# Kernel tuning notes

Measured on AMD Instinct MI355X. Metric: run time of the kernel, lower is better.

## Reference

```python
import jax, jax.numpy as jnp
import numpy as np

D_MODEL = 768
N_HEADS = 12
HEAD_DIM = D_MODEL // N_HEADS


def setup_inputs() -> dict:
    key = jax.random.key(0)
    ks = jax.random.split(key, 9)
    s = 1.0 / np.sqrt(D_MODEL)
    inp = {
        "inputs": jax.random.normal(ks[0], (1, 4096, D_MODEL), dtype=jnp.float32),
        "Wq": jax.random.uniform(ks[1], (D_MODEL, D_MODEL), jnp.float32, -s, s),
        "bq": jax.random.uniform(ks[2], (D_MODEL,), jnp.float32, -s, s),
        "Wk": jax.random.uniform(ks[3], (D_MODEL, D_MODEL), jnp.float32, -s, s),
        "bk": jax.random.uniform(ks[4], (D_MODEL,), jnp.float32, -s, s),
        "Wv": jax.random.uniform(ks[5], (D_MODEL, D_MODEL), jnp.float32, -s, s),
        "bv": jax.random.uniform(ks[6], (D_MODEL,), jnp.float32, -s, s),
        "Wo": jax.random.uniform(ks[7], (D_MODEL, D_MODEL), jnp.float32, -s, s),
        "bo": jax.random.uniform(ks[8], (D_MODEL,), jnp.float32, -s, s),
    }
    return inp


def reference(inputs, Wq, bq, Wk, bk, Wv, bv, Wo, bo):
    B, S, D = inputs.shape
    H, Hd = N_HEADS, HEAD_DIM

    def split_heads(x):  # [B,S,D] -> [B,H,S,Hd]
        return x.reshape(B, S, H, Hd).transpose(0, 2, 1, 3)

    # nn.Linear computes x @ W.T + b
    Q = split_heads(inputs @ Wq.T + bq)
    K = split_heads(inputs @ Wk.T + bk)
    V = split_heads(inputs @ Wv.T + bv)

    scores = jnp.einsum("bhsd,bhtd->bhst", Q, K) / jnp.sqrt(jnp.float32(Hd))
    causal = jnp.tril(jnp.ones((S, S), dtype=bool))  # True = keep
    scores = jnp.where(causal, scores, -jnp.inf)
    attn = jax.nn.softmax(scores, axis=-1)  # dropout is identity in eval

    out = jnp.einsum("bhst,bhtd->bhsd", attn, V)
    out = out.transpose(0, 2, 1, 3).reshape(B, S, D)
    return out @ Wo.T + bo
```

## Files before the change

kernel.cpp:

```cpp
#include <hip/hip_runtime.h>
#include <stdint.h>

#define SEQ 4096
#define DM 768
#define NH 12
#define HD 64

typedef unsigned short u16;
typedef short short8 __attribute__((ext_vector_type(8)));
typedef float floatx4 __attribute__((ext_vector_type(4)));
typedef float floatx16 __attribute__((ext_vector_type(16)));
typedef u16 u16x4 __attribute__((ext_vector_type(4)));

__device__ inline u16 f2b(float f) {
  union { float f; uint32_t u; } v; v.f = f;
  uint32_t u = v.u;
  return (u16)((u + 0x7fffu + ((u >> 16) & 1u)) >> 16);
}

__device__ inline float b2f(u16 x) {
  union { uint32_t u; float f; } v; v.u = ((uint32_t)x) << 16;
  return v.f;
}

#if defined(__has_builtin)
#if __has_builtin(__builtin_amdgcn_cvt_pk_bf16_f32)
#define HAVE_PK_BF16 1
#endif
#endif

__device__ inline uint32_t pk_bf16(float a, float b) {
#ifdef HAVE_PK_BF16
  typedef __bf16 bf16x2_t __attribute__((ext_vector_type(2)));
  union { bf16x2_t v; uint32_t u; } c;
  c.v = __builtin_amdgcn_cvt_pk_bf16_f32(a, b);
  return c.u;
#else
  uint32_t r;
  asm("v_cvt_pk_bf16_f32 %0, %1, %2" : "=v"(r) : "v"(a), "v"(b));
  return r;
#endif
}

__device__ inline void pl32swap(uint32_t& a, uint32_t& b) {
  asm("v_permlane32_swap_b32 %0, %1" : "+v"(a), "+v"(b));
}

__device__ inline void load_lds16(const void* g, void* l) {
  __builtin_amdgcn_global_load_lds(
      (const __attribute__((address_space(1))) uint32_t*)g,
      (__attribute__((address_space(3))) uint32_t*)l, 16, 0, 0);
}

__global__ __launch_bounds__(256) void convert_all(
    const float* __restrict__ X, const float* __restrict__ Wq,
    const float* __restrict__ Wk, const float* __restrict__ Wv,
    const float* __restrict__ Wo,
    u16* __restrict__ Xb, u16* __restrict__ Wqb, u16* __restrict__ Wkb,
    u16* __restrict__ Wvb, u16* __restrict__ Wob) {
  int t = blockIdx.x * 256 + threadIdx.x;
  const int NX = SEQ * DM / 4;
  const int NW = DM * DM / 4;
  const float* src; u16* dst; int off;
  if (t < NX)               { src = X;  dst = Xb;  off = t; }
  else if (t < NX + NW)     { src = Wq; dst = Wqb; off = t - NX; }
  else if (t < NX + 2 * NW) { src = Wk; dst = Wkb; off = t - NX - NW; }
  else if (t < NX + 3 * NW) { src = Wv; dst = Wvb; off = t - NX - 2 * NW; }
  else if (t < NX + 4 * NW) { src = Wo; dst = Wob; off = t - NX - 3 * NW; }
  else return;
  float4 v = *(const float4*)(src + (size_t)off * 4);
  uint2 o;
  o.x = pk_bf16(v.x, v.y);
  o.y = pk_bf16(v.z, v.w);
  *(uint2*)(dst + (size_t)off * 4) = o;
}

__global__ __launch_bounds__(256) void gemm_qkv(
    const u16* __restrict__ Xb,
    const u16* __restrict__ Wqb, const u16* __restrict__ Wkb,
    const u16* __restrict__ Wvb,
    const float* __restrict__ bq, const float* __restrict__ bk,
    const float* __restrict__ bv,
    u16* __restrict__ Qh, u16* __restrict__ Kh, u16* __restrict__ VtG) {
  const u16* W; const float* bias;
  const int z = blockIdx.z;
  if (z == 0)      { W = Wqb; bias = bq; }
  else if (z == 1) { W = Wkb; bias = bk; }
  else             { W = Wvb; bias = bv; }

  __shared__ u16 smem[16384];

  const int tid = threadIdx.x;
  const int wave = tid >> 6, lane = tid & 63;
  const int g = lane >> 4, ln = lane & 15;
  const int m0 = blockIdx.y * 64, n0 = blockIdx.x * 64;
  const int wm = (wave & 1) * 32, wn = (wave >> 1) * 32;
  const int srow = lane >> 3;
  const int schunk = (lane & 7) ^ srow;
  const int swz = ln & 7;

  floatx4 acc[2][2] = {};

#pragma unroll
  for (int i = 0; i < 2; ++i) {
    int u = wave * 2 + i;
    load_lds16(Xb + (size_t)(m0 + u * 8 + srow) * DM + schunk * 8, smem + u * 512);
    load_lds16(W + (size_t)(n0 + u * 8 + srow) * DM + schunk * 8,
               smem + 8192 + u * 512);
  }

  for (int kt = 0; kt < 12; ++kt) {
    const int cur = kt & 1;
    __syncthreads();
    if (kt < 11) {
      const int k0 = (kt + 1) * 64, nb = cur ^ 1;
#pragma unroll
      for (int i = 0; i < 2; ++i) {
        int u = wave * 2 + i;
        load_lds16(Xb + (size_t)(m0 + u * 8 + srow) * DM + k0 + schunk * 8,
                   smem + nb * 4096 + u * 512);
        load_lds16(W + (size_t)(n0 + u * 8 + srow) * DM + k0 + schunk * 8,
                   smem + 8192 + nb * 4096 + u * 512);
      }
    }
    const u16* Ac = smem + cur * 4096;
    const u16* Bc = smem + 8192 + cur * 4096;
    short8 af[2][2], bf[2][2];
#pragma unroll
    for (int mi = 0; mi < 2; ++mi)
#pragma unroll
      for (int kh = 0; kh < 2; ++kh)
        af[mi][kh] = *(const short8*)(Ac + (wm + mi * 16 + ln) * 64 +
                                      ((kh * 4 + g) ^ swz) * 8);
#pragma unroll
    for (int ni = 0; ni < 2; ++ni)
#pragma unroll
      for (int kh = 0; kh < 2; ++kh)
        bf[ni][kh] = *(const short8*)(Bc + (wn + ni * 16 + ln) * 64 +
                                      ((kh * 4 + g) ^ swz) * 8);
#pragma unroll
    for (int kh = 0; kh < 2; ++kh)
#pragma unroll
      for (int mi = 0; mi < 2; ++mi)
#pragma unroll
        for (int ni = 0; ni < 2; ++ni)
          acc[mi][ni] = __builtin_amdgcn_mfma_f32_16x16x32_bf16(
              af[mi][kh], bf[ni][kh], acc[mi][ni], 0, 0, 0);
  }

  const float qscale = 0.125f * 1.44269504089f;
  const int hh = n0 >> 6;
  __syncthreads();

  if (z == 2) {
#pragma unroll
    for (int mi = 0; mi < 2; ++mi) {
      int row0 = wm + mi * 16 + g * 4;
#pragma unroll
      for (int ni = 0; ni < 2; ++ni) {
        int col = wn + ni * 16 + ln;
        float b = bias[n0 + col];
        uint2 o;
        o.x = pk_bf16(acc[mi][ni][0] + b, acc[mi][ni][1] + b);
        o.y = pk_bf16(acc[mi][ni][2] + b, acc[mi][ni][3] + b);
        *(uint2*)(smem + col * 72 + row0) = o;
      }
    }
    __syncthreads();
#pragma unroll
    for (int t = 0; t < 2; ++t) {
      int unit = tid + t * 256;
      int dcol = unit >> 3, ch = unit & 7;
      short8 v = *(const short8*)(smem + dcol * 72 + ch * 8);
      *(short8*)(VtG + ((size_t)(hh * 64 + dcol)) * SEQ + m0 + ch * 8) = v;
    }
  } else {
    u16* out = (z == 0) ? Qh : Kh;
    float cs = (z == 0) ? qscale : 1.0f;
#pragma unroll
    for (int mi = 0; mi < 2; ++mi) {
      int row0 = wm + mi * 16 + g * 4;
#pragma unroll
      for (int ni = 0; ni < 2; ++ni) {
        int col = wn + ni * 16 + ln;
        float b = bias[n0 + col];
        uint32_t w0 = pk_bf16((acc[mi][ni][0] + b) * cs, (acc[mi][ni][1] + b) * cs);
        uint32_t w1 = pk_bf16((acc[mi][ni][2] + b) * cs, (acc[mi][ni][3] + b) * cs);
        smem[(row0 + 0) * 72 + col] = (u16)w0;
        smem[(row0 + 1) * 72 + col] = (u16)(w0 >> 16);
        smem[(row0 + 2) * 72 + col] = (u16)w1;
        smem[(row0 + 3) * 72 + col] = (u16)(w1 >> 16);
      }
    }
    __syncthreads();
#pragma unroll
    for (int t = 0; t < 2; ++t) {
      int unit = tid + t * 256;
      int row = unit >> 3, ch = unit & 7;
      short8 v = *(const short8*)(smem + row * 72 + ch * 8);
      *(short8*)(out + ((size_t)hh * SEQ + m0 + row) * HD + ch * 8) = v;
    }
  }
}

#define CHUNK 8
#define M0 40.0f
__global__ __launch_bounds__(256, 4) void attn_chunk(
    const u16* __restrict__ Qh, const u16* __restrict__ Kh,
    const u16* __restrict__ VtG, u16* __restrict__ Opart,
    float* __restrict__ Lp) {
  const int p = blockIdx.y * NH + blockIdx.x;
  const int slot = p % 24, cyc = p / 24;
  const int qq = 3 * (slot & 7) + (slot >> 3);
  const int h = qq >> 1;
  const int j = cyc * 2 + (qq & 1);
  const int r = 143 - j;
  int g = 0;
#pragma unroll
  for (int t = 1; t < 8; ++t)
    if (2 * t * (t + 1) <= r) g = t;
  const int gp1 = g + 1;
  const int rr = r - 2 * g * gp1;
  const int dq = rr / gp1;
  const int qB = 4 * g + dq;
  const int ci = rr - dq * gp1;
  const int kb0 = ci * CHUNK;
  const int kb1 = min(kb0 + CHUNK, 2 * qB + 2);
  const int slot2 = h * 144 + gp1 * (2 * g + (qB & 3)) + ci;

  const int tid = threadIdx.x, wave = tid >> 6, lane = tid & 63;
  const int hi = lane >> 5, lq = lane & 31;
  const int q0 = qB * 128;
  const int qwave = q0 + wave * 32;
  const int srow = lane >> 3;
  const int schunk = (lane & 7) ^ srow;
  const int rsw = lane & 7;

  __shared__ u16 Ks[2 * 4096];
  __shared__ u16 Vt[2 * 4096];

  const int qglob = qwave + lq;
  const u16* Qbase = Qh + ((size_t)h * SEQ + qglob) * HD;
  short8 aq[4];
#pragma unroll
  for (int s = 0; s < 4; ++s)
    aq[s] = *(const short8*)(Qbase + s * 16 + hi * 8);

  floatx16 oacc[2] = {};
  floatx4 lacc = {};

  const size_t kbase = (size_t)h * SEQ * HD;
  const size_t vbase = (size_t)h * 64 * SEQ;

  auto stage = [&](int kbIdx, int buf) {
#pragma unroll
    for (int i = 0; i < 2; ++i) {
      int u = wave * 2 + i;
      load_lds16(Kh + kbase + (size_t)(kbIdx * 64 + u * 8 + srow) * HD + schunk * 8,
                 Ks + buf * 4096 + u * 512);
      load_lds16(VtG + vbase + (size_t)(u * 8 + srow) * SEQ + kbIdx * 64 + schunk * 8,
                 Vt + buf * 4096 + u * 512);
    }
  };

  stage(kb0, 0);

  for (int kb = kb0; kb < kb1; ++kb) {
    const int cur = (kb - kb0) & 1;
    __syncthreads();
    if (kb + 1 < kb1) stage(kb + 1, cur ^ 1);

    const u16* Kc = Ks + cur * 4096;
    const u16* Vc = Vt + cur * 4096;

    if (kb * 64 > qwave + 31) continue;

    floatx16 st[2];
#pragma unroll
    for (int kblk = 0; kblk < 2; ++kblk)
#pragma unroll
      for (int r2 = 0; r2 < 16; ++r2) st[kblk][r2] = -M0;
    __builtin_amdgcn_s_setprio(1);
#pragma unroll
    for (int s = 0; s < 4; ++s)
#pragma unroll
      for (int kblk = 0; kblk < 2; ++kblk) {
        short8 kf = *(const short8*)(Kc + (kblk * 32 + lq) * 64 +
                                     ((s * 2 + hi) ^ rsw) * 8);
        st[kblk] = __builtin_amdgcn_mfma_f32_32x32x16_bf16(kf, aq[s], st[kblk],
                                                           0, 0, 0);
      }
    __builtin_amdgcn_s_setprio(0);

    if (kb * 64 + 63 > qwave) {
#pragma unroll
      for (int kblk = 0; kblk < 2; ++kblk)
#pragma unroll
        for (int r2 = 0; r2 < 16; ++r2) {
          int key = kb * 64 + kblk * 32 + (r2 & 3) + 8 * (r2 >> 2) + 4 * hi;
          if (key > qglob) st[kblk][r2] = -1e30f;
        }
    }

    uint32_t w[2][8];
#pragma unroll
    for (int kblk = 0; kblk < 2; ++kblk) {
#pragma unroll
      for (int r2 = 0; r2 < 16; ++r2)
        st[kblk][r2] = __builtin_amdgcn_exp2f(st[kblk][r2]);
#pragma unroll
      for (int r2 = 0; r2 < 4; ++r2)
        lacc[r2] += st[kblk][r2] + st[kblk][4 + r2] + st[kblk][8 + r2] +
                    st[kblk][12 + r2];
#pragma unroll
      for (int i = 0; i < 8; ++i)
        w[kblk][i] = pk_bf16(st[kblk][2 * i], st[kblk][2 * i + 1]);
    }

    __builtin_amdgcn_s_setprio(1);
#pragma unroll
    for (int ks = 0; ks < 4; ++ks) {
      const int kblk = ks >> 1, base = (ks & 1) * 4;
      uint32_t d0 = w[kblk][base + 0], d2 = w[kblk][base + 2];
      uint32_t d1 = w[kblk][base + 1], d3 = w[kblk][base + 3];
      pl32swap(d0, d2);
      pl32swap(d1, d3);
      union { uint32_t u[4]; short8 s; } bp;
      bp.u[0] = d0; bp.u[1] = d1; bp.u[2] = d2; bp.u[3] = d3;
#pragma unroll
      for (int dblk = 0; dblk < 2; ++dblk) {
        short8 vf = *(const short8*)(Vc + (dblk * 32 + lq) * 64 +
                                     ((ks * 2 + hi) ^ rsw) * 8);
        oacc[dblk] = __builtin_amdgcn_mfma_f32_32x32x16_bf16(vf, bp.s, oacc[dblk],
                                                             0, 0, 0);
      }
    }
    __builtin_amdgcn_s_setprio(0);
  }

  float l_i = lacc[0] + lacc[1] + lacc[2] + lacc[3];
  l_i += __shfl_xor(l_i, 32);

  float inv = 1.f / l_i;
  int qloc = wave * 32 + lq;
  u16* Op = Opart + (size_t)slot2 * 8192 + qloc * 64;
#pragma unroll
  for (int dblk = 0; dblk < 2; ++dblk)
#pragma unroll
    for (int qd = 0; qd < 4; ++qd) {
      uint2 o;
      o.x = pk_bf16(oacc[dblk][qd * 4 + 0] * inv, oacc[dblk][qd * 4 + 1] * inv);
      o.y = pk_bf16(oacc[dblk][qd * 4 + 2] * inv, oacc[dblk][qd * 4 + 3] * inv);
      *(uint2*)(Op + dblk * 32 + qd * 8 + hi * 4) = o;
    }
  if (hi == 0) Lp[(size_t)slot2 * 128 + qloc] = l_i;
}

__global__ __launch_bounds__(256) void attn_merge(
    const u16* __restrict__ Opart, const float* __restrict__ Lp,
    u16* __restrict__ Ob) {
  const int h = blockIdx.x, qB = blockIdx.y;
  const int g = qB >> 2;
  const int n = g + 1;
  const int base = h * 144 + (g + 1) * (2 * g + (qB & 3));
  const int q = threadIdx.x >> 1;
  const int d0 = (threadIdx.x & 1) * 32;

  float L = 0.f;
  for (int i = 0; i < n; ++i) L += Lp[(size_t)(base + i) * 128 + q];
  float invL = 1.f / L;

  float acc[32];
#pragma unroll
  for (int jj = 0; jj < 32; ++jj) acc[jj] = 0.f;
  for (int i = 0; i < n; ++i) {
    float wi = Lp[(size_t)(base + i) * 128 + q] * invL;
    const u16* src = Opart + (size_t)(base + i) * 8192 + q * 64 + d0;
#pragma unroll
    for (int c = 0; c < 4; ++c) {
      short8 a = ((const short8*)src)[c];
#pragma unroll
      for (int jj = 0; jj < 8; ++jj) acc[c * 8 + jj] += wi * b2f((u16)a[jj]);
    }
  }

  u16* dst = Ob + (size_t)(qB * 128 + q) * DM + h * HD + d0;
#pragma unroll
  for (int c = 0; c < 4; ++c) {
    uint4 o;
    o.x = pk_bf16(acc[c * 8 + 0], acc[c * 8 + 1]);
    o.y = pk_bf16(acc[c * 8 + 2], acc[c * 8 + 3]);
    o.z = pk_bf16(acc[c * 8 + 4], acc[c * 8 + 5]);
    o.w = pk_bf16(acc[c * 8 + 6], acc[c * 8 + 7]);
    ((uint4*)dst)[c] = o;
  }
}

__global__ __launch_bounds__(256) void gemm_out(
    const u16* __restrict__ Ab, const u16* __restrict__ Wob,
    const float* __restrict__ bo, float* __restrict__ Cout) {
  __shared__ u16 smem[16384];

  const int tid = threadIdx.x;
  const int wave = tid >> 6, lane = tid & 63;
  const int g = lane >> 4, ln = lane & 15;
  const int m0 = blockIdx.y * 64, n0 = blockIdx.x * 64;
  const int wm = (wave & 1) * 32, wn = (wave >> 1) * 32;
  const int srow = lane >> 3;
  const int schunk = (lane & 7) ^ srow;
  const int swz = ln & 7;

  floatx4 acc[2][2] = {};

#pragma unroll
  for (int i = 0; i < 2; ++i) {
    int u = wave * 2 + i;
    load_lds16(Ab + (size_t)(m0 + u * 8 + srow) * DM + schunk * 8, smem + u * 512);
    load_lds16(Wob + (size_t)(n0 + u * 8 + srow) * DM + schunk * 8,
               smem + 8192 + u * 512);
  }

  for (int kt = 0; kt < 12; ++kt) {
    const int cur = kt & 1;
    __syncthreads();
    if (kt < 11) {
      const int k0 = (kt + 1) * 64, nb = cur ^ 1;
#pragma unroll
      for (int i = 0; i < 2; ++i) {
        int u = wave * 2 + i;
        load_lds16(Ab + (size_t)(m0 + u * 8 + srow) * DM + k0 + schunk * 8,
                   smem + nb * 4096 + u * 512);
        load_lds16(Wob + (size_t)(n0 + u * 8 + srow) * DM + k0 + schunk * 8,
                   smem + 8192 + nb * 4096 + u * 512);
      }
    }
    const u16* Ac = smem + cur * 4096;
    const u16* Bc = smem + 8192 + cur * 4096;
    short8 af[2][2], bf[2][2];
#pragma unroll
    for (int mi = 0; mi < 2; ++mi)
#pragma unroll
      for (int kh = 0; kh < 2; ++kh)
        af[mi][kh] = *(const short8*)(Ac + (wm + mi * 16 + ln) * 64 +
                                      ((kh * 4 + g) ^ swz) * 8);
#pragma unroll
    for (int ni = 0; ni < 2; ++ni)
#pragma unroll
      for (int kh = 0; kh < 2; ++kh)
        bf[ni][kh] = *(const short8*)(Bc + (wn + ni * 16 + ln) * 64 +
                                      ((kh * 4 + g) ^ swz) * 8);
#pragma unroll
    for (int kh = 0; kh < 2; ++kh)
#pragma unroll
      for (int mi = 0; mi < 2; ++mi)
#pragma unroll
        for (int ni = 0; ni < 2; ++ni)
          acc[mi][ni] = __builtin_amdgcn_mfma_f32_16x16x32_bf16(
              af[mi][kh], bf[ni][kh], acc[mi][ni], 0, 0, 0);
  }

#pragma unroll
  for (int mi = 0; mi < 2; ++mi) {
    int row = m0 + wm + mi * 16 + g * 4;
#pragma unroll
    for (int ni = 0; ni < 2; ++ni) {
      int col = n0 + wn + ni * 16 + ln;
      float b = bo[col];
#pragma unroll
      for (int r = 0; r < 4; ++r)
        Cout[(size_t)(row + r) * DM + col] = acc[mi][ni][r] + b;
    }
  }
}

extern "C" void kernel_launch(void* const* d_in, const int* in_sizes, int n_in,
                              void* d_out, int out_size, void* d_ws, size_t ws_size,
                              hipStream_t stream) {
  const float* X  = (const float*)d_in[0];
  const float* Wq = (const float*)d_in[1];
  const float* bq = (const float*)d_in[2];
  const float* Wk = (const float*)d_in[3];
  const float* bk = (const float*)d_in[4];
  const float* Wv = (const float*)d_in[5];
  const float* bv = (const float*)d_in[6];
  const float* Wo = (const float*)d_in[7];
  const float* bo = (const float*)d_in[8];
  float* out = (float*)d_out;

  char* ws = (char*)d_ws;
  u16* Wob = (u16*)ws; ws += (size_t)DM * DM * 2;
  u16* Qh  = (u16*)ws; ws += (size_t)NH * SEQ * HD * 2;
  u16* Kh  = (u16*)ws; ws += (size_t)NH * SEQ * HD * 2;
  u16* VtG = (u16*)ws; ws += (size_t)NH * SEQ * HD * 2;
  u16* Ob  = (u16*)ws; ws += (size_t)SEQ * DM * 2;
  float* Lp = (float*)ws; ws += (size_t)NH * 144 * 128 * 4;
  char* ovl = ws;
  u16* Xb  = (u16*)ovl;
  u16* Wqb = Xb + (size_t)SEQ * DM;
  u16* Wkb = Wqb + (size_t)DM * DM;
  u16* Wvb = Wkb + (size_t)DM * DM;
  u16* Opart = (u16*)ovl;

  convert_all<<<5376, 256, 0, stream>>>(X, Wq, Wk, Wv, Wo, Xb, Wqb, Wkb, Wvb, Wob);

  dim3 gq(DM / 64, SEQ / 64, 3);
  gemm_qkv<<<gq, 256, 0, stream>>>(Xb, Wqb, Wkb, Wvb, bq, bk, bv, Qh, Kh, VtG);

  dim3 ga(NH, 144);
  attn_chunk<<<ga, 256, 0, stream>>>(Qh, Kh, VtG, Opart, Lp);

  dim3 gm(NH, 32);
  attn_merge<<<gm, 256, 0, stream>>>(Opart, Lp, Ob);

  dim3 go(DM / 64, SEQ / 64);
  gemm_out<<<go, 256, 0, stream>>>(Ob, Wob, bo, out);
}
```

Baseline: 175.8 us.

## Enlarge GEMM tiles to 128x64 with 2 waves and double attention key chunk

```diff
diff --git a/kernel.cpp b/kernel.cpp
--- a/kernel.cpp
+++ b/kernel.cpp
@@ -10,7 +10,6 @@
 typedef short short8 __attribute__((ext_vector_type(8)));
 typedef float floatx4 __attribute__((ext_vector_type(4)));
 typedef float floatx16 __attribute__((ext_vector_type(16)));
-typedef u16 u16x4 __attribute__((ext_vector_type(4)));
 
 __device__ inline u16 f2b(float f) {
   union { float f; uint32_t u; } v; v.f = f;
@@ -75,7 +74,7 @@
   *(uint2*)(dst + (size_t)off * 4) = o;
 }
 
-__global__ __launch_bounds__(256) void gemm_qkv(
+__global__ __launch_bounds__(128) void gemm_qkv(
     const u16* __restrict__ Xb,
     const u16* __restrict__ Wqb, const u16* __restrict__ Wkb,
     const u16* __restrict__ Wvb,
@@ -88,122 +87,120 @@
   else if (z == 1) { W = Wkb; bias = bk; }
   else             { W = Wvb; bias = bv; }
 
-  __shared__ u16 smem[16384];
+  __shared__ u16 As[2 * 8192];
+  __shared__ u16 Bs[2 * 4096];
 
   const int tid = threadIdx.x;
   const int wave = tid >> 6, lane = tid & 63;
   const int g = lane >> 4, ln = lane & 15;
-  const int m0 = blockIdx.y * 64, n0 = blockIdx.x * 64;
-  const int wm = (wave & 1) * 32, wn = (wave >> 1) * 32;
+  const int m0 = blockIdx.y * 128, n0 = blockIdx.x * 64;
   const int srow = lane >> 3;
   const int schunk = (lane & 7) ^ srow;
   const int swz = ln & 7;
 
-  floatx4 acc[2][2] = {};
-
-#pragma unroll
-  for (int i = 0; i < 2; ++i) {
-    int u = wave * 2 + i;
-    load_lds16(Xb + (size_t)(m0 + u * 8 + srow) * DM + schunk * 8, smem + u * 512);
-    load_lds16(W + (size_t)(n0 + u * 8 + srow) * DM + schunk * 8,
-               smem + 8192 + u * 512);
-  }
+  floatx4 acc[4][4] = {};
+
+  auto stage = [&](int k0, int buf) {
+#pragma unroll
+    for (int i = 0; i < 8; ++i) {
+      int u = wave * 8 + i;
+      load_lds16(Xb + (size_t)(m0 + u * 8 + srow) * DM + k0 + schunk * 8,
+                 As + buf * 8192 + u * 512);
+    }
+#pragma unroll
+    for (int i = 0; i < 4; ++i) {
+      int u = wave * 4 + i;
+      load_lds16(W + (size_t)(n0 + u * 8 + srow) * DM + k0 + schunk * 8,
+                 Bs + buf * 4096 + u * 512);
+    }
+  };
+
+  stage(0, 0);
 
   for (int kt = 0; kt < 12; ++kt) {
     const int cur = kt & 1;
     __syncthreads();
-    if (kt < 11) {
-      const int k0 = (kt + 1) * 64, nb = cur ^ 1;
-#pragma unroll
-      for (int i = 0; i < 2; ++i) {
-        int u = wave * 2 + i;
-        load_lds16(Xb + (size_t)(m0 + u * 8 + srow) * DM + k0 + schunk * 8,
-                   smem + nb * 4096 + u * 512);
-        load_lds16(W + (size_t)(n0 + u * 8 + srow) * DM + k0 + schunk * 8,
-                   smem + 8192 + nb * 4096 + u * 512);
-      }
-    }
-    const u16* Ac = smem + cur * 4096;
-    const u16* Bc = smem + 8192 + cur * 4096;
-    short8 af[2][2], bf[2][2];
-#pragma unroll
-    for (int mi = 0; mi < 2; ++mi)
-#pragma unroll
-      for (int kh = 0; kh < 2; ++kh)
-        af[mi][kh] = *(const short8*)(Ac + (wm + mi * 16 + ln) * 64 +
-                                      ((kh * 4 + g) ^ swz) * 8);
-#pragma unroll
-    for (int ni = 0; ni < 2; ++ni)
-#pragma unroll
-      for (int kh = 0; kh < 2; ++kh)
-        bf[ni][kh] = *(const short8*)(Bc + (wn + ni * 16 + ln) * 64 +
-                                      ((kh * 4 + g) ^ swz) * 8);
-#pragma unroll
-    for (int kh = 0; kh < 2; ++kh)
-#pragma unroll
-      for (int mi = 0; mi < 2; ++mi)
-#pragma unroll
-        for (int ni = 0; ni < 2; ++ni)
+    if (kt < 11) stage((kt + 1) * 64, cur ^ 1);
+    const u16* Ac = As + cur * 8192;
+    const u16* Bc = Bs + cur * 4096;
+#pragma unroll
+    for (int kh = 0; kh < 2; ++kh) {
+      short8 af[4], bf[4];
+#pragma unroll
+      for (int mi = 0; mi < 4; ++mi)
+        af[mi] = *(const short8*)(Ac + (wave * 64 + mi * 16 + ln) * 64 +
+                                  ((kh * 4 + g) ^ swz) * 8);
+#pragma unroll
+      for (int ni = 0; ni < 4; ++ni)
+        bf[ni] = *(const short8*)(Bc + (ni * 16 + ln) * 64 +
+                                  ((kh * 4 + g) ^ swz) * 8);
+#pragma unroll
+      for (int mi = 0; mi < 4; ++mi)
+#pragma unroll
+        for (int ni = 0; ni < 4; ++ni)
           acc[mi][ni] = __builtin_amdgcn_mfma_f32_16x16x32_bf16(
-              af[mi][kh], bf[ni][kh], acc[mi][ni], 0, 0, 0);
+              af[mi], bf[ni], acc[mi][ni], 0, 0, 0);
+    }
   }
 
   const float qscale = 0.125f * 1.44269504089f;
-  const int hh = n0 >> 6;
+  const int hh = blockIdx.x;
   __syncthreads();
 
   if (z == 2) {
-#pragma unroll
-    for (int mi = 0; mi < 2; ++mi) {
-      int row0 = wm + mi * 16 + g * 4;
-#pragma unroll
-      for (int ni = 0; ni < 2; ++ni) {
-        int col = wn + ni * 16 + ln;
+    u16* ep = (u16*)As;
+#pragma unroll
+    for (int mi = 0; mi < 4; ++mi) {
+      int row0 = wave * 64 + mi * 16 + g * 4;
+#pragma unroll
+      for (int ni = 0; ni < 4; ++ni) {
+        int col = ni * 16 + ln;
         float b = bias[n0 + col];
         uint2 o;
         o.x = pk_bf16(acc[mi][ni][0] + b, acc[mi][ni][1] + b);
         o.y = pk_bf16(acc[mi][ni][2] + b, acc[mi][ni][3] + b);
-        *(uint2*)(smem + col * 72 + row0) = o;
+        *(uint2*)(ep + col * 136 + row0) = o;
       }
     }
     __syncthreads();
 #pragma unroll
-    for (int t = 0; t < 2; ++t) {
-      int unit = tid + t * 256;
-      int dcol = unit >> 3, ch = unit & 7;
-      short8 v = *(const short8*)(smem + dcol * 72 + ch * 8);
+    for (int t = 0; t < 8; ++t) {
+      int unit = tid + t * 128;
+      int dcol = unit >> 4, ch = unit & 15;
+      short8 v = *(const short8*)(ep + dcol * 136 + ch * 8);
       *(short8*)(VtG + ((size_t)(hh * 64 + dcol)) * SEQ + m0 + ch * 8) = v;
     }
   } else {
+    u16* ep = (u16*)As;
     u16* out = (z == 0) ? Qh : Kh;
     float cs = (z == 0) ? qscale : 1.0f;
 #pragma unroll
-    for (int mi = 0; mi < 2; ++mi) {
-      int row0 = wm + mi * 16 + g * 4;
-#pragma unroll
-      for (int ni = 0; ni < 2; ++ni) {
-        int col = wn + ni * 16 + ln;
+    for (int mi = 0; mi < 4; ++mi) {
+      int row0 = wave * 64 + mi * 16 + g * 4;
+#pragma unroll
+      for (int ni = 0; ni < 4; ++ni) {
+        int col = ni * 16 + ln;
         float b = bias[n0 + col];
         uint32_t w0 = pk_bf16((acc[mi][ni][0] + b) * cs, (acc[mi][ni][1] + b) * cs);
         uint32_t w1 = pk_bf16((acc[mi][ni][2] + b) * cs, (acc[mi][ni][3] + b) * cs);
-        smem[(row0 + 0) * 72 + col] = (u16)w0;
-        smem[(row0 + 1) * 72 + col] = (u16)(w0 >> 16);
-        smem[(row0 + 2) * 72 + col] = (u16)w1;
-        smem[(row0 + 3) * 72 + col] = (u16)(w1 >> 16);
+        ep[(row0 + 0) * 72 + col] = (u16)w0;
+        ep[(row0 + 1) * 72 + col] = (u16)(w0 >> 16);
+        ep[(row0 + 2) * 72 + col] = (u16)w1;
+        ep[(row0 + 3) * 72 + col] = (u16)(w1 >> 16);
       }
     }
     __syncthreads();
 #pragma unroll
-    for (int t = 0; t < 2; ++t) {
-      int unit = tid + t * 256;
+    for (int t = 0; t < 8; ++t) {
+      int unit = tid + t * 128;
       int row = unit >> 3, ch = unit & 7;
-      short8 v = *(const short8*)(smem + row * 72 + ch * 8);
+      short8 v = *(const short8*)(ep + row * 72 + ch * 8);
       *(short8*)(out + ((size_t)hh * SEQ + m0 + row) * HD + ch * 8) = v;
     }
   }
 }
 
-#define CHUNK 8
+#define CHUNK 16
 #define M0 40.0f
 __global__ __launch_bounds__(256, 4) void attn_chunk(
     const u16* __restrict__ Qh, const u16* __restrict__ Kh,
@@ -213,20 +210,15 @@
   const int slot = p % 24, cyc = p / 24;
   const int qq = 3 * (slot & 7) + (slot >> 3);
   const int h = qq >> 1;
-  const int j = cyc * 2 + (qq & 1);
-  const int r = 143 - j;
-  int g = 0;
-#pragma unroll
-  for (int t = 1; t < 8; ++t)
-    if (2 * t * (t + 1) <= r) g = t;
-  const int gp1 = g + 1;
-  const int rr = r - 2 * g * gp1;
-  const int dq = rr / gp1;
-  const int qB = 4 * g + dq;
-  const int ci = rr - dq * gp1;
+  const int b = 79 - (cyc * 2 + (qq & 1));
+  int qB, ci;
+  if (b < 8)       { qB = b;               ci = 0; }
+  else if (b < 24) { int r = b - 8;  qB = 8 + (r >> 1); ci = r & 1; }
+  else if (b < 48) { int r = b - 24; int d = r / 3; qB = 16 + d; ci = r - d * 3; }
+  else             { int r = b - 48; qB = 24 + (r >> 2); ci = r & 3; }
   const int kb0 = ci * CHUNK;
   const int kb1 = min(kb0 + CHUNK, 2 * qB + 2);
-  const int slot2 = h * 144 + gp1 * (2 * g + (qB & 3)) + ci;
+  const int slot2 = (h * 32 + qB) * 4 + ci;
 
   const int tid = threadIdx.x, wave = tid >> 6, lane = tid & 63;
   const int hi = lane >> 5, lq = lane & 31;
@@ -360,9 +352,8 @@
     const u16* __restrict__ Opart, const float* __restrict__ Lp,
     u16* __restrict__ Ob) {
   const int h = blockIdx.x, qB = blockIdx.y;
-  const int g = qB >> 2;
-  const int n = g + 1;
-  const int base = h * 144 + (g + 1) * (2 * g + (qB & 3));
+  const int n = (qB >> 3) + 1;
+  const int base = (h * 32 + qB) * 4;
   const int q = threadIdx.x >> 1;
   const int d0 = (threadIdx.x & 1) * 32;
 
@@ -396,75 +387,71 @@
   }
 }
 
-__global__ __launch_bounds__(256) void gemm_out(
+__global__ __launch_bounds__(128) void gemm_out(
     const u16* __restrict__ Ab, const u16* __restrict__ Wob,
     const float* __restrict__ bo, float* __restrict__ Cout) {
-  __shared__ u16 smem[16384];
+  __shared__ u16 As[2 * 8192];
+  __shared__ u16 Bs[2 * 4096];
 
   const int tid = threadIdx.x;
   const int wave = tid >> 6, lane = tid & 63;
   const int g = lane >> 4, ln = lane & 15;
-  const int m0 = blockIdx.y * 64, n0 = blockIdx.x * 64;
-  const int wm = (wave & 1) * 32, wn = (wave >> 1) * 32;
+  const int m0 = blockIdx.y * 128, n0 = blockIdx.x * 64;
   const int srow = lane >> 3;
   const int schunk = (lane & 7) ^ srow;
   const int swz = ln & 7;
 
-  floatx4 acc[2][2] = {};
-
-#pragma unroll
-  for (int i = 0; i < 2; ++i) {
-    int u = wave * 2 + i;
-    load_lds16(Ab + (size_t)(m0 + u * 8 + srow) * DM + schunk * 8, smem + u * 512);
-    load_lds16(Wob + (size_t)(n0 + u * 8 + srow) * DM + schunk * 8,
-               smem + 8192 + u * 512);
-  }
+  floatx4 acc[4][4] = {};
+
+  auto stage = [&](int k0, int buf) {
+#pragma unroll
+    for (int i = 0; i < 8; ++i) {
+      int u = wave * 8 + i;
+      load_lds16(Ab + (size_t)(m0 + u * 8 + srow) * DM + k0 + schunk * 8,
+                 As + buf * 8192 + u * 512);
+    }
+#pragma unroll
+    for (int i = 0; i < 4; ++i) {
+      int u = wave * 4 + i;
+      load_lds16(Wob + (size_t)(n0 + u * 8 + srow) * DM + k0 + schunk * 8,
+                 Bs + buf * 4096 + u * 512);
+    }
+  };
+
+  stage(0, 0);
 
   for (int kt = 0; kt < 12; ++kt) {
     const int cur = kt & 1;
     __syncthreads();
-    if (kt < 11) {
-      const int k0 = (kt + 1) * 64, nb = cur ^ 1;
-#pragma unroll
-      for (int i = 0; i < 2; ++i) {
-        int u = wave * 2 + i;
-        load_lds16(Ab + (size_t)(m0 + u * 8 + srow) * DM + k0 + schunk * 8,
-                   smem + nb * 4096 + u * 512);
-        load_lds16(Wob + (size_t)(n0 + u * 8 + srow) * DM + k0 + schunk * 8,
-                   smem + 8192 + nb * 4096 + u * 512);
-      }
-    }
-    const u16* Ac = smem + cur * 4096;
-    const u16* Bc = smem + 8192 + cur * 4096;
-    short8 af[2][2], bf[2][2];
-#pragma unroll
-    for (int mi = 0; mi < 2; ++mi)
-#pragma unroll
-      for (int kh = 0; kh < 2; ++kh)
-        af[mi][kh] = *(const short8*)(Ac + (wm + mi * 16 + ln) * 64 +
-                                      ((kh * 4 + g) ^ swz) * 8);
-#pragma unroll
-    for (int ni = 0; ni < 2; ++ni)
-#pragma unroll
-      for (int kh = 0; kh < 2; ++kh)
-        bf[ni][kh] = *(const short8*)(Bc + (wn + ni * 16 + ln) * 64 +
-                                      ((kh * 4 + g) ^ swz) * 8);
-#pragma unroll
-    for (int kh = 0; kh < 2; ++kh)
-#pragma unroll
-      for (int mi = 0; mi < 2; ++mi)
-#pragma unroll
-        for (int ni = 0; ni < 2; ++ni)
+    if (kt < 11) stage((kt + 1) * 64, cur ^ 1);
+    const u16* Ac = As + cur * 8192;
+    const u16* Bc = Bs + cur * 4096;
+#pragma unroll
+    for (int kh = 0; kh < 2; ++kh) {
+      short8 af[4], bf[4];
+#pragma unroll
+      for (int mi = 0; mi < 4; ++mi)
+        af[mi] = *(const short8*)(Ac + (wave * 64 + mi * 16 + ln) * 64 +
+                                  ((kh * 4 + g) ^ swz) * 8);
+#pragma unroll
+      for (int ni = 0; ni < 4; ++ni)
+        bf[ni] = *(const short8*)(Bc + (ni * 16 + ln) * 64 +
+                                  ((kh * 4 + g) ^ swz) * 8);
+#pragma unroll
+      for (int mi = 0; mi < 4; ++mi)
+#pragma unroll
+        for (int ni = 0; ni < 4; ++ni)
           acc[mi][ni] = __builtin_amdgcn_mfma_f32_16x16x32_bf16(
-              af[mi][kh], bf[ni][kh], acc[mi][ni], 0, 0, 0);
-  }
-
-#pragma unroll
-  for (int mi = 0; mi < 2; ++mi) {
-    int row = m0 + wm + mi * 16 + g * 4;
-#pragma unroll
-    for (int ni = 0; ni < 2; ++ni) {
-      int col = n0 + wn + ni * 16 + ln;
+              af[mi], bf[ni], acc[mi][ni], 0, 0, 0);
+    }
+  }
+
+#pragma unroll
+  for (int mi = 0; mi < 4; ++mi) {
+    int row = m0 + wave * 64 + mi * 16 + g * 4;
+#pragma unroll
+    for (int ni = 0; ni < 4; ++ni) {
+      int col = n0 + ni * 16 + ln;
       float b = bo[col];
 #pragma unroll
       for (int r = 0; r < 4; ++r)
@@ -493,7 +480,7 @@
   u16* Kh  = (u16*)ws; ws += (size_t)NH * SEQ * HD * 2;
   u16* VtG = (u16*)ws; ws += (size_t)NH * SEQ * HD * 2;
   u16* Ob  = (u16*)ws; ws += (size_t)SEQ * DM * 2;
-  float* Lp = (float*)ws; ws += (size_t)NH * 144 * 128 * 4;
+  float* Lp = (float*)ws; ws += (size_t)NH * 32 * 4 * 128 * 4;
   char* ovl = ws;
   u16* Xb  = (u16*)ovl;
   u16* Wqb = Xb + (size_t)SEQ * DM;
@@ -503,15 +490,15 @@
 
   convert_all<<<5376, 256, 0, stream>>>(X, Wq, Wk, Wv, Wo, Xb, Wqb, Wkb, Wvb, Wob);
 
-  dim3 gq(DM / 64, SEQ / 64, 3);
-  gemm_qkv<<<gq, 256, 0, stream>>>(Xb, Wqb, Wkb, Wvb, bq, bk, bv, Qh, Kh, VtG);
-
-  dim3 ga(NH, 144);
+  dim3 gq(DM / 64, SEQ / 128, 3);
+  gemm_qkv<<<gq, 128, 0, stream>>>(Xb, Wqb, Wkb, Wvb, bq, bk, bv, Qh, Kh, VtG);
+
+  dim3 ga(NH, 80);
   attn_chunk<<<ga, 256, 0, stream>>>(Qh, Kh, VtG, Opart, Lp);
 
   dim3 gm(NH, 32);
   attn_merge<<<gm, 256, 0, stream>>>(Opart, Lp, Ob);
 
-  dim3 go(DM / 64, SEQ / 64);
-  gemm_out<<<go, 256, 0, stream>>>(Ob, Wob, bo, out);
-}
+  dim3 go(DM / 64, SEQ / 128);
+  gemm_out<<<go, 128, 0, stream>>>(Ob, Wob, bo, out);
+}
```

Result: slower. 180.8 us (+2.8%).
